# Kernel optimization log

Hardware: AMD Instinct MI355X
Metric: run time of the kernel (lower is better)

The kernel has to match this reference:

```python
import jax, jax.numpy as jnp
import numpy as np

CTX = 77; WIDTH = 512; HEADS = 8; LAYERS = 12; EMBED = 1024; VOCAB = 49408
N = 128; P = 8; LP = 16; EOT = 49407


def _ln(x, w, b, eps=1e-5):
    m = jnp.mean(x, axis=-1, keepdims=True)
    v = jnp.var(x, axis=-1, keepdims=True)
    return (x - m) * jax.lax.rsqrt(v + eps) * w + b


def setup_inputs() -> dict:
    key = jax.random.key(0)
    ks = jax.random.split(key, 12)
    # tokens strictly below EOT, then place exactly one EOT at a valid position (<= CTX-LP)
    text = jax.random.randint(ks[0], (N, CTX), 0, EOT)
    eot_pos = jax.random.randint(ks[1], (N,), 5, CTX - LP + 1)
    text = text.at[jnp.arange(N), eot_pos].set(EOT)
    s = 0.02
    return {
        "text": text,
        "context_prompt": jax.random.normal(ks[2], (P, LP, WIDTH)) * s,
        "tok_emb": jax.random.normal(ks[3], (VOCAB, WIDTH)) * s,
        "pos_emb": jax.random.normal(ks[4], (CTX, WIDTH)) * 0.01,
        "qkv_w": jax.random.normal(ks[5], (LAYERS, 3 * WIDTH, WIDTH)) * s,
        "qkv_b": jnp.zeros((LAYERS, 3 * WIDTH)),
        "out_w": jax.random.normal(ks[6], (LAYERS, WIDTH, WIDTH)) * s,
        "out_b": jnp.zeros((LAYERS, WIDTH)),
        "ln1_w": jnp.ones((LAYERS, WIDTH)),
        "ln1_b": jnp.zeros((LAYERS, WIDTH)),
        "ln2_w": jnp.ones((LAYERS, WIDTH)),
        "ln2_b": jnp.zeros((LAYERS, WIDTH)),
        "fc_w": jax.random.normal(ks[7], (LAYERS, 4 * WIDTH, WIDTH)) * s,
        "fc_b": jnp.zeros((LAYERS, 4 * WIDTH)),
        "proj_w": jax.random.normal(ks[8], (LAYERS, WIDTH, 4 * WIDTH)) * s,
        "proj_b": jnp.zeros((LAYERS, WIDTH)),
        "lnf_w": jnp.ones((WIDTH,)),
        "lnf_b": jnp.zeros((WIDTH,)),
        "text_projection": jax.random.normal(ks[9], (WIDTH, EMBED)) * s,
    }


def _encode(text, context_prompt, tok_emb, pos_emb, qkv_w, qkv_b, out_w, out_b,
            ln1_w, ln1_b, ln2_w, ln2_b, fc_w, fc_b, proj_w, proj_b,
            lnf_w, lnf_b, text_projection):
    pos_y = jnp.argmax(text == EOT, axis=1)                       # [N] first EOT per sample
    x = tok_emb[text]                                             # [N,L,D]
    t = jnp.arange(CTX)
    # vectorized per-sample insertion: out[t] = x[t] for t<pos_y; prompt[t-pos_y] for
    # pos_y<=t<pos_y+LP; x[t-LP+1] otherwise (matches the torch concat semantics)
    src = jnp.where(t[None] < pos_y[:, None], t[None], t[None] - LP + 1)
    src = jnp.clip(src, 0, CTX - 1)
    base = jnp.take_along_axis(x, src[:, :, None], axis=1)        # [N,L,D]
    in_prompt = (t[None] >= pos_y[:, None]) & (t[None] < pos_y[:, None] + LP)
    pidx = jnp.clip(t[None] - pos_y[:, None], 0, LP - 1)          # [N,L]
    prom = context_prompt[:, pidx, :]                             # [P,N,L,D]
    xn = jnp.where(in_prompt[None, :, :, None], prom, base[None]) + pos_emb
    B = P * N
    xn = xn.reshape(B, CTX, WIDTH)

    dh = WIDTH // HEADS
    scale = 1.0 / float(np.sqrt(dh))
    mask = jnp.triu(jnp.full((CTX, CTX), -jnp.inf, xn.dtype), 1)  # causal attn_mask

    def block(h, p):
        qw, qb, ow, ob, l1w, l1b, l2w, l2b, fw, fb, pw, pb = p
        y = _ln(h, l1w, l1b)
        qkv = y @ qw.T + qb
        q, k, v = jnp.split(qkv, 3, axis=-1)
        q = q.reshape(B, CTX, HEADS, dh)
        k = k.reshape(B, CTX, HEADS, dh)
        v = v.reshape(B, CTX, HEADS, dh)
        sc = jnp.einsum('blhd,bmhd->bhlm', q, k) * scale + mask
        a = jax.nn.softmax(sc, axis=-1)
        o = jnp.einsum('bhlm,bmhd->blhd', a, v).reshape(B, CTX, WIDTH)
        h = h + o @ ow.T + ob
        y = _ln(h, l2w, l2b)
        u = y @ fw.T + fb
        u = u * jax.nn.sigmoid(1.702 * u)                         # QuickGELU (CLIP)
        h = h + u @ pw.T + pb
        return h, None

    xn, _ = jax.lax.scan(block, xn, (qkv_w, qkv_b, out_w, out_b, ln1_w, ln1_b,
                                     ln2_w, ln2_b, fc_w, fc_b, proj_w, proj_b))
    xn = _ln(xn, lnf_w, lnf_b).reshape(P, N, CTX, WIDTH)
    take = (pos_y + LP - 1)[None, :, None, None]                  # shifted EOT position
    feats = jnp.take_along_axis(xn, jnp.broadcast_to(take, (P, N, 1, WIDTH)), axis=2)[:, :, 0, :]
    feats = feats @ text_projection                               # [P,N,E]
    feats = feats / jnp.linalg.norm(feats, axis=-1, keepdims=True)
    feats = jnp.mean(feats, axis=1, keepdims=True)                # [P,1,E]
    feats = feats / jnp.linalg.norm(feats, axis=-1, keepdims=True)
    return feats


def reference(text, context_prompt, tok_emb, pos_emb, qkv_w, qkv_b, out_w, out_b,
              ln1_w, ln1_b, ln2_w, ln2_b, fc_w, fc_b, proj_w, proj_b,
              lnf_w, lnf_b, text_projection):
    return _encode(text, context_prompt, tok_emb, pos_emb, qkv_w, qkv_b, out_w, out_b,
                   ln1_w, ln1_b, ln2_w, ln2_b, fc_w, fc_b, proj_w, proj_b,
                   lnf_w, lnf_b, text_projection)
```

## Files before the change

### kernel.cpp

```cpp
#include <hip/hip_runtime.h>
#include <math.h>
#include <stdint.h>

#define CTX 77
#define WIDTH 512
#define HEADS 8
#define DH 64
#define LAYERS 12
#define EMBED 1024
#define NTXT 128
#define PP 8
#define LPROMPT 16
#define EOTTOK 49407
#define BSEQ (PP*NTXT)
#define ROWS (BSEQ*CTX)

typedef unsigned short ushort_t;
typedef __attribute__((ext_vector_type(8))) short short8;
typedef __attribute__((ext_vector_type(4))) float floatx4;

__device__ __forceinline__ float b2f(ushort_t u){
  union { unsigned int i; float f; } x; x.i = ((unsigned int)u) << 16; return x.f;
}
__device__ __forceinline__ ushort_t f2b(float f){
  union { float f; unsigned int i; } x; x.f = f;
  unsigned int r = x.i + 0x7fffu + ((x.i >> 16) & 1u);
  return (ushort_t)(r >> 16);
}
__device__ __forceinline__ float wsum(float v){
  #pragma unroll
  for (int o = 32; o > 0; o >>= 1) v += __shfl_xor(v, o, 64);
  return v;
}
__device__ __forceinline__ float wmax(float v){
  #pragma unroll
  for (int o = 32; o > 0; o >>= 1) v = fmaxf(v, __shfl_xor(v, o, 64));
  return v;
}

__device__ __forceinline__ void async16(const void* g, void* l){
  __builtin_amdgcn_global_load_lds(
      (const __attribute__((address_space(1))) void*)(uintptr_t)g,
      (__attribute__((address_space(3))) void*)(uint32_t)(uintptr_t)l,
      16, 0, 0);
}

__global__ __launch_bounds__(256) void k_conv(
    const float* __restrict__ s, ushort_t* __restrict__ d, int n4)
{
  int i = blockIdx.x * 256 + threadIdx.x;
  if (i < n4){
    float4 v = ((const float4*)s)[i];
    ushort_t o[4] = { f2b(v.x), f2b(v.y), f2b(v.z), f2b(v.w) };
    ((int2*)d)[i] = *(int2*)o;
  }
}

__global__ void k_posy(const int* __restrict__ text, int* __restrict__ posy){
  int n = threadIdx.x;
  if (n < NTXT){
    int p = 0;
    for (int t = 0; t < CTX; ++t){ if (text[n*CTX + t] == EOTTOK){ p = t; break; } }
    posy[n] = p;
  }
}

template<bool RF32>
__global__ __launch_bounds__(256) void k_embed(
    const int* __restrict__ text, const float* __restrict__ cprompt,
    const float* __restrict__ tok_emb, const float* __restrict__ pos_emb,
    const int* __restrict__ posy, void* __restrict__ Hp)
{
  long long idx = (long long)blockIdx.x * 256 + threadIdx.x;
  int d   = (int)(idx & 511);
  int row = (int)(idx >> 9);
  int t  = row % CTX;
  int pn = row / CTX;
  int n  = pn % NTXT;
  int p  = pn / NTXT;
  int py = posy[n];
  float v;
  if (t >= py && t < py + LPROMPT){
    int pidx = t - py;
    v = cprompt[(p*LPROMPT + pidx)*WIDTH + d];
  } else {
    int src = (t < py) ? t : (t - LPROMPT + 1);
    src = min(max(src, 0), CTX-1);
    int tok = text[n*CTX + src];
    v = tok_emb[(long long)tok*WIDTH + d];
  }
  v += pos_emb[t*WIDTH + d];
  if constexpr (RF32) ((float*)Hp)[idx] = v;
  else                ((ushort_t*)Hp)[idx] = f2b(v);
}

template<bool RF32>
__global__ __launch_bounds__(256) void k_ln(
    const void* __restrict__ Hp, const float* __restrict__ w,
    const float* __restrict__ b, ushort_t* __restrict__ Y, int nrows)
{
  int wid = threadIdx.x >> 6, lane = threadIdx.x & 63;
  int row = blockIdx.x * 4 + wid;
  if (row >= nrows) return;
  float v[8];
  if constexpr (RF32){
    const float* x = (const float*)Hp + (long long)row * WIDTH;
    #pragma unroll
    for (int i = 0; i < 8; ++i) v[i] = x[lane*8 + i];
  } else {
    const ushort_t* x = (const ushort_t*)Hp + (long long)row * WIDTH;
    int4 raw = *(const int4*)(x + lane*8);
    ushort_t* u = (ushort_t*)&raw;
    #pragma unroll
    for (int i = 0; i < 8; ++i) v[i] = b2f(u[i]);
  }
  float s = 0.f, ss = 0.f;
  #pragma unroll
  for (int i = 0; i < 8; ++i){ s += v[i]; ss += v[i]*v[i]; }
  s = wsum(s); ss = wsum(ss);
  float mean = s * (1.0f/WIDTH);
  float var  = ss * (1.0f/WIDTH) - mean*mean;
  float rs = rsqrtf(var + 1e-5f);
  ushort_t o[8];
  #pragma unroll
  for (int i = 0; i < 8; ++i){
    int d = lane*8 + i;
    o[i] = f2b((v[i]-mean)*rs*w[d] + b[d]);
  }
  *(int4*)(Y + (long long)row*WIDTH + lane*8) = *(int4*)o;
}

template<int MODE, bool RF32>
__global__ __launch_bounds__(256) void k_gemm(
    const ushort_t* __restrict__ A, const ushort_t* __restrict__ W,
    const float* __restrict__ bias, void* __restrict__ Hp,
    ushort_t* __restrict__ O, int K, int N)
{
  __shared__ ushort_t As[128*64];
  __shared__ ushort_t Bs[128*64];
  int tid  = threadIdx.x;
  int lane = tid & 63, wid = tid >> 6;
  int wm = wid >> 1, wn = wid & 1;
  long long m0 = (long long)blockIdx.y * 128;
  int n0 = blockIdx.x * 128;

  floatx4 acc[4][4];
  #pragma unroll
  for (int i = 0; i < 4; ++i)
    #pragma unroll
    for (int j = 0; j < 4; ++j){ floatx4 z = {0.f,0.f,0.f,0.f}; acc[i][j] = z; }

  const int srow = tid >> 3;
  const int sc8  = ((tid ^ (tid >> 3)) & 7) * 8;
  const ushort_t* gA = A + (m0 + srow) * (long long)K + sc8;
  const ushort_t* gB = W + ((size_t)n0 + srow) * K + sc8;
  const size_t qstep = (size_t)32 * K;
  const int lbase = wid * 512;

  const int quad = lane >> 4, r = lane & 15;
  const int swz = (r & 7) * 8;

  for (int k0 = 0; k0 < K; k0 += 64){
    __syncthreads();
    #pragma unroll
    for (int q = 0; q < 4; ++q){
      async16(gA + q*qstep, As + q*2048 + lbase);
      async16(gB + q*qstep, Bs + q*2048 + lbase);
    }
    gA += 64; gB += 64;
    __syncthreads();
    #pragma unroll
    for (int s = 0; s < 2; ++s){
      const int co = (s*32 + quad*8) ^ swz;
      short8 af[4], bf[4];
      #pragma unroll
      for (int i = 0; i < 4; ++i) af[i] = *(const short8*)(As + (wm*64 + i*16 + r)*64 + co);
      #pragma unroll
      for (int j = 0; j < 4; ++j) bf[j] = *(const short8*)(Bs + (wn*64 + j*16 + r)*64 + co);
      #pragma unroll
      for (int i = 0; i < 4; ++i)
        #pragma unroll
        for (int j = 0; j < 4; ++j)
          acc[i][j] = __builtin_amdgcn_mfma_f32_16x16x32_bf16(af[i], bf[j], acc[i][j], 0, 0, 0);
    }
  }

  int cn = lane & 15;
  #pragma unroll
  for (int i = 0; i < 4; ++i){
    #pragma unroll
    for (int j = 0; j < 4; ++j){
      int gcol = n0 + wn*64 + j*16 + cn;
      float bv = bias[gcol];
      #pragma unroll
      for (int rg = 0; rg < 4; ++rg){
        long long grow = m0 + wm*64 + i*16 + quad*4 + rg;
        float v = acc[i][j][rg] + bv;
        if (MODE == 0){
          O[grow*N + gcol] = f2b(v);
        } else if (MODE == 1){
          float g = v / (1.0f + __expf(-1.702f*v));
          O[grow*N + gcol] = f2b(g);
        } else {
          long long idx = grow*N + gcol;
          if constexpr (RF32) ((float*)Hp)[idx] += v;
          else { ushort_t* hb = (ushort_t*)Hp; hb[idx] = f2b(b2f(hb[idx]) + v); }
        }
      }
    }
  }
}

__global__ __launch_bounds__(256) void k_attn(
    const ushort_t* __restrict__ QKV, ushort_t* __restrict__ Y)
{
  __shared__ char smem[55872];
  ushort_t* Qs = (ushort_t*)smem;
  ushort_t* Ks = (ushort_t*)(smem + 11520);
  float*    Ss = (float*)smem;
  ushort_t* Vt = (ushort_t*)(smem + 25920);
  ushort_t* Ps = (ushort_t*)(smem + 39232);

  int b = blockIdx.x >> 3, h = blockIdx.x & 7;
  int tid = threadIdx.x;
  int lane = tid & 63, wid = tid >> 6;
  int quad = lane >> 4, r = lane & 15;
  const ushort_t* base = QKV + (size_t)b*CTX*1536 + h*64;

  #pragma unroll
  for (int it = 0; it < 5; ++it){
    int id = tid + it*256;
    int t  = id >> 4;
    int d4 = (id & 15) * 4;
    ushort_t q[4], k[4], v[4];
    if (t < CTX){
      const ushort_t* rp = base + (size_t)t*1536 + d4;
      *(int2*)q = *(const int2*)(rp);
      *(int2*)k = *(const int2*)(rp + 512);
      *(int2*)v = *(const int2*)(rp + 1024);
    } else {
      q[0]=q[1]=q[2]=q[3]=0; k[0]=k[1]=k[2]=k[3]=0; v[0]=v[1]=v[2]=v[3]=0;
    }
    *(int2*)(Qs + t*72 + d4) = *(int2*)q;
    *(int2*)(Ks + t*72 + d4) = *(int2*)k;
    #pragma unroll
    for (int i = 0; i < 4; ++i) Vt[(d4+i)*104 + t] = v[i];
  }
  {
    int z = tid * 4;
    int d = z >> 4, c = 80 + (z & 15);
    ushort_t zz[4] = {0,0,0,0};
    *(int2*)(Vt + d*104 + c) = *(int2*)zz;
  }
  __syncthreads();

  const int TI[15] = {0,1,1,2,2,2,3,3,3,3,4,4,4,4,4};
  const int TJ[15] = {0,0,1,0,1,2,0,1,2,3,0,1,2,3,4};
  floatx4 cS[4];
  int ntile = 0;
  for (int tt = wid; tt < 15; tt += 4, ++ntile){
    int i = TI[tt], j = TJ[tt];
    floatx4 c = {0.f,0.f,0.f,0.f};
    #pragma unroll
    for (int s = 0; s < 2; ++s){
      short8 aq = *(const short8*)(Qs + (i*16 + r)*72 + s*32 + quad*8);
      short8 bk = *(const short8*)(Ks + (j*16 + r)*72 + s*32 + quad*8);
      c = __builtin_amdgcn_mfma_f32_16x16x32_bf16(aq, bk, c, 0, 0, 0);
    }
    cS[ntile] = c;
  }
  __syncthreads();

  {
    int idx = 0;
    for (int tt = wid; tt < 15; tt += 4, ++idx){
      int i = TI[tt], j = TJ[tt];
      #pragma unroll
      for (int rg = 0; rg < 4; ++rg){
        int q  = i*16 + quad*4 + rg;
        int kk = j*16 + r;
        float s = cS[idx][rg] * 0.125f;
        if (kk > q) s = -1e30f;
        Ss[q*81 + kk] = s;
      }
    }
  }
  __syncthreads();

  for (int q = wid; q < 80; q += 4){
    if (q >= CTX){
      Ps[q*104 + lane] = 0;
      if (lane < 32) Ps[q*104 + 64 + lane] = 0;
      continue;
    }
    int k1 = 64 + lane;
    float s0 = (lane <= q) ? Ss[q*81 + lane] : -1e30f;
    float s1 = (k1  <= q) ? Ss[q*81 + k1 ]  : -1e30f;
    float mx = wmax(fmaxf(s0, s1));
    float e0 = (lane <= q) ? __expf(s0 - mx) : 0.0f;
    float e1 = (k1  <= q) ? __expf(s1 - mx) : 0.0f;
    float inv = 1.0f / wsum(e0 + e1);
    Ps[q*104 + lane] = f2b(e0 * inv);
    if (lane < 32) Ps[q*104 + 64 + lane] = f2b(e1 * inv);
  }
  __syncthreads();

  for (int tt = wid; tt < 20; tt += 4){
    int mi = tt >> 2, ni = tt & 3;
    floatx4 c = {0.f,0.f,0.f,0.f};
    #pragma unroll
    for (int kc = 0; kc < 3; ++kc){
      short8 ap = *(const short8*)(Ps + (mi*16 + r)*104 + kc*32 + quad*8);
      short8 bv = *(const short8*)(Vt + (ni*16 + r)*104 + kc*32 + quad*8);
      c = __builtin_amdgcn_mfma_f32_16x16x32_bf16(ap, bv, c, 0, 0, 0);
    }
    #pragma unroll
    for (int rg = 0; rg < 4; ++rg){
      int q = mi*16 + quad*4 + rg;
      if (q < CTX)
        Y[((size_t)b*CTX + q)*WIDTH + h*64 + ni*16 + r] = f2b(c[rg]);
    }
  }
}

template<bool RF32>
__global__ __launch_bounds__(256) void k_lnf_gather(
    const void* __restrict__ Hp, const int* __restrict__ posy,
    const float* __restrict__ w, const float* __restrict__ b,
    ushort_t* __restrict__ FI)
{
  int wid = threadIdx.x >> 6, lane = threadIdx.x & 63;
  int rr = blockIdx.x * 4 + wid;
  if (rr >= BSEQ) return;
  int n = rr % NTXT;
  int tok = posy[n] + LPROMPT - 1;
  long long row = (long long)rr*CTX + tok;
  float v[8];
  if constexpr (RF32){
    const float* x = (const float*)Hp + row * WIDTH;
    #pragma unroll
    for (int i = 0; i < 8; ++i) v[i] = x[lane*8 + i];
  } else {
    const ushort_t* x = (const ushort_t*)Hp + row * WIDTH;
    int4 raw = *(const int4*)(x + lane*8);
    ushort_t* u = (ushort_t*)&raw;
    #pragma unroll
    for (int i = 0; i < 8; ++i) v[i] = b2f(u[i]);
  }
  float s = 0.f, ss = 0.f;
  #pragma unroll
  for (int i = 0; i < 8; ++i){ s += v[i]; ss += v[i]*v[i]; }
  s = wsum(s); ss = wsum(ss);
  float mean = s * (1.0f/WIDTH);
  float var  = ss * (1.0f/WIDTH) - mean*mean;
  float rs = rsqrtf(var + 1e-5f);
  ushort_t o[8];
  #pragma unroll
  for (int i = 0; i < 8; ++i){
    int d = lane*8 + i;
    o[i] = f2b((v[i]-mean)*rs*w[d] + b[d]);
  }
  *(int4*)(FI + (long long)rr*WIDTH + lane*8) = *(int4*)o;
}

__global__ __launch_bounds__(256) void k_fproj(
    const ushort_t* __restrict__ FI, const float* __restrict__ TP,
    float* __restrict__ F)
{
  int idx = blockIdx.x * 256 + threadIdx.x;
  int e = idx & (EMBED-1);
  int m = idx >> 10;
  float acc = 0.f;
  #pragma unroll 8
  for (int k = 0; k < WIDTH; ++k)
    acc += b2f(FI[m*WIDTH + k]) * TP[k*EMBED + e];
  F[idx] = acc;
}

__global__ __launch_bounds__(256) void k_rownorm(float* __restrict__ F)
{
  __shared__ float red[4];
  int rr = blockIdx.x;
  float* x = F + (long long)rr*EMBED;
  float ss = 0.f;
  for (int i = threadIdx.x; i < EMBED; i += 256){ float v = x[i]; ss += v*v; }
  ss = wsum(ss);
  int wid = threadIdx.x >> 6, lane = threadIdx.x & 63;
  if (lane == 0) red[wid] = ss;
  __syncthreads();
  float inv = rsqrtf(red[0]+red[1]+red[2]+red[3]);
  for (int i = threadIdx.x; i < EMBED; i += 256) x[i] *= inv;
}

__global__ __launch_bounds__(256) void k_meannorm(
    const float* __restrict__ F, float* __restrict__ OUT)
{
  __shared__ float red[4];
  int p = blockIdx.x;
  float m[4]; float ss = 0.f;
  #pragma unroll
  for (int j = 0; j < 4; ++j){
    int e = threadIdx.x + j*256;
    float s = 0.f;
    for (int n = 0; n < NTXT; ++n) s += F[((long long)(p*NTXT + n))*EMBED + e];
    s *= (1.0f/NTXT);
    m[j] = s; ss += s*s;
  }
  ss = wsum(ss);
  int wid = threadIdx.x >> 6, lane = threadIdx.x & 63;
  if (lane == 0) red[wid] = ss;
  __syncthreads();
  float inv = rsqrtf(red[0]+red[1]+red[2]+red[3]);
  #pragma unroll
  for (int j = 0; j < 4; ++j)
    OUT[p*EMBED + threadIdx.x + j*256] = m[j]*inv;
}


template<bool RF32>
static void run_all(const int* text, const float* cprompt, const float* tok_emb,
                    const float* pos_emb,
                    const ushort_t* Wqkv, const float* qkv_b,
                    const ushort_t* Wout, const float* out_b,
                    const float* ln1_w, const float* ln1_b,
                    const float* ln2_w, const float* ln2_b,
                    const ushort_t* Wfc, const float* fc_b,
                    const ushort_t* Wproj, const float* proj_b,
                    const float* lnf_w, const float* lnf_b, const float* tproj,
                    int* posy, void* H, ushort_t* Y, ushort_t* BIG,
                    ushort_t* FI, float* F, float* OUT, int sc, hipStream_t stream)
{
  const int rows_c = ROWS / sc;
  const int seqs_c = BSEQ / sc;

  k_posy<<<1, 128, 0, stream>>>(text, posy);
  k_embed<RF32><<<(ROWS*512)/256, 256, 0, stream>>>(text, cprompt, tok_emb, pos_emb, posy, H);

  for (int L = 0; L < LAYERS; ++L){
    k_ln<RF32><<<ROWS/4, 256, 0, stream>>>(H, ln1_w + L*WIDTH, ln1_b + L*WIDTH, Y, ROWS);
    for (int c = 0; c < sc; ++c){
      size_t r0 = (size_t)c * rows_c;
      k_gemm<0,RF32><<<dim3(12, rows_c/128), 256, 0, stream>>>(
          Y + r0*WIDTH, Wqkv + (size_t)L*1536*512, qkv_b + L*1536,
          nullptr, BIG, 512, 1536);
      k_attn<<<seqs_c*HEADS, 256, 0, stream>>>(BIG, Y + r0*WIDTH);
    }
    k_gemm<2,RF32><<<dim3(4, ROWS/128), 256, 0, stream>>>(
        Y, Wout + (size_t)L*512*512, out_b + L*512, H, nullptr, 512, 512);
    k_ln<RF32><<<ROWS/4, 256, 0, stream>>>(H, ln2_w + L*WIDTH, ln2_b + L*WIDTH, Y, ROWS);
    for (int c = 0; c < sc; ++c){
      size_t r0 = (size_t)c * rows_c;
      void* Hoff = RF32 ? (void*)((float*)H + r0*WIDTH) : (void*)((ushort_t*)H + r0*WIDTH);
      k_gemm<1,RF32><<<dim3(16, rows_c/128), 256, 0, stream>>>(
          Y + r0*WIDTH, Wfc + (size_t)L*2048*512, fc_b + L*2048,
          nullptr, BIG, 512, 2048);
      k_gemm<2,RF32><<<dim3(4, rows_c/128), 256, 0, stream>>>(
          BIG, Wproj + (size_t)L*512*2048, proj_b + L*512, Hoff, nullptr, 2048, 512);
    }
  }

  k_lnf_gather<RF32><<<BSEQ/4, 256, 0, stream>>>(H, posy, lnf_w, lnf_b, FI);
  k_fproj<<<(BSEQ*EMBED)/256, 256, 0, stream>>>(FI, tproj, F);
  k_rownorm<<<BSEQ, 256, 0, stream>>>(F);
  k_meannorm<<<PP, 256, 0, stream>>>(F, OUT);
}

extern "C" void kernel_launch(void* const* d_in, const int* in_sizes, int n_in,
                              void* d_out, int out_size, void* d_ws, size_t ws_size,
                              hipStream_t stream)
{
  const int*   text    = (const int*)d_in[0];
  const float* cprompt = (const float*)d_in[1];
  const float* tok_emb = (const float*)d_in[2];
  const float* pos_emb = (const float*)d_in[3];
  const float* qkv_w   = (const float*)d_in[4];
  const float* qkv_b   = (const float*)d_in[5];
  const float* out_w   = (const float*)d_in[6];
  const float* out_b   = (const float*)d_in[7];
  const float* ln1_w   = (const float*)d_in[8];
  const float* ln1_b   = (const float*)d_in[9];
  const float* ln2_w   = (const float*)d_in[10];
  const float* ln2_b   = (const float*)d_in[11];
  const float* fc_w    = (const float*)d_in[12];
  const float* fc_b    = (const float*)d_in[13];
  const float* proj_w  = (const float*)d_in[14];
  const float* proj_b  = (const float*)d_in[15];
  const float* lnf_w   = (const float*)d_in[16];
  const float* lnf_b   = (const float*)d_in[17];
  const float* tproj   = (const float*)d_in[18];

  const size_t nQKV = (size_t)LAYERS*1536*512;
  const size_t nOUT = (size_t)LAYERS*512*512;
  const size_t nFC  = (size_t)LAYERS*2048*512;
  const size_t nPRJ = (size_t)LAYERS*512*2048;
  const size_t nWB  = nQKV + nOUT + nFC + nPRJ;

  auto al = [](size_t b){ return (b + 255) & ~(size_t)255; };
  const size_t fixed = al(NTXT*sizeof(int)) + al((size_t)ROWS*WIDTH*2 )
                     + al((size_t)BSEQ*WIDTH*2 ) + al((size_t)BSEQ*EMBED*4 )
                     + al(nWB*2);
  int sc = 8; bool hf32 = false;
  const int scs[4] = {1, 2, 4, 8};
  bool found = false;
  for (int pass = 0; pass < 2 && !found; ++pass){
    size_t hbytes = (size_t)ROWS*WIDTH*(pass == 0 ? 4 : 2);
    for (int i = 0; i < 4; ++i){
      size_t big = (size_t)(ROWS/scs[i]) * 2048 * 2;
      if (fixed + al(hbytes) + al(big) <= ws_size){
        sc = scs[i]; hf32 = (pass == 0); found = true; break;
      }
    }
  }

  char* ws = (char*)d_ws;
  size_t off = 0;
  auto alloc = [&](size_t bytes)->char*{
    char* pp = ws + off; off += (bytes + 255) & ~(size_t)255; return pp;
  };
  int*      posy = (int*)     alloc(NTXT*sizeof(int));
  void*     H    = (void*)    alloc((size_t)ROWS*WIDTH*(hf32 ? 4 : 2));
  ushort_t* Y    = (ushort_t*)alloc((size_t)ROWS*WIDTH*2);
  ushort_t* BIG  = (ushort_t*)alloc((size_t)(ROWS/sc)*2048*2);
  ushort_t* FI   = (ushort_t*)alloc((size_t)BSEQ*WIDTH*2);
  float*    F    = (float*)   alloc((size_t)BSEQ*EMBED*4);
  ushort_t* WB   = (ushort_t*)alloc(nWB*2);
  ushort_t* Wqkv = WB;
  ushort_t* Wout = WB + nQKV;
  ushort_t* Wfc  = WB + nQKV + nOUT;
  ushort_t* Wprj = WB + nQKV + nOUT + nFC;

  k_conv<<<(int)((nQKV/4 + 255)/256), 256, 0, stream>>>(qkv_w,  Wqkv, (int)(nQKV/4));
  k_conv<<<(int)((nOUT/4 + 255)/256), 256, 0, stream>>>(out_w,  Wout, (int)(nOUT/4));
  k_conv<<<(int)((nFC /4 + 255)/256), 256, 0, stream>>>(fc_w,   Wfc,  (int)(nFC /4));
  k_conv<<<(int)((nPRJ/4 + 255)/256), 256, 0, stream>>>(proj_w, Wprj, (int)(nPRJ/4));

  if (hf32)
    run_all<true >(text, cprompt, tok_emb, pos_emb, Wqkv, qkv_b, Wout, out_b,
                   ln1_w, ln1_b, ln2_w, ln2_b, Wfc, fc_b, Wprj, proj_b,
                   lnf_w, lnf_b, tproj, posy, H, Y, BIG, FI, F,
                   (float*)d_out, sc, stream);
  else
    run_all<false>(text, cprompt, tok_emb, pos_emb, Wqkv, qkv_b, Wout, out_b,
                   ln1_w, ln1_b, ln2_w, ln2_b, Wfc, fc_b, Wprj, proj_b,
                   lnf_w, lnf_b, tproj, posy, H, Y, BIG, FI, F,
                   (float*)d_out, sc, stream);
}
```

Baseline: 17.50 ms.

## Vectorize embedding, shrink attention LDS, add occupancy hints, force chunked scheduling

The embedding kernel now has each thread handle eight contiguous elements using float4 loads and wide stores instead of one scalar element per thread. The attention kernel's score buffer is packed to a 77-column stride and padding rows are no longer written, which reduces LDS use so more blocks can fit per CU (launch bounds now request 3). The GEMM gets a min-blocks-per-CU launch bound of 4, which may force register limits and spills. Workspace selection now allows only 4 or 8 sequence chunks, so the intermediate buffer stays smaller and more cache-resident, at the cost of more kernel launches.

Result: faster. 15.05 ms (-14.0%).

```diff
diff --git a/kernel.cpp b/kernel.cpp
--- a/kernel.cpp
+++ b/kernel.cpp
@@ -72,26 +72,41 @@
     const int* __restrict__ posy, void* __restrict__ Hp)
 {
   long long idx = (long long)blockIdx.x * 256 + threadIdx.x;
-  int d   = (int)(idx & 511);
-  int row = (int)(idx >> 9);
+  int d8  = (int)(idx & 63) * 8;
+  int row = (int)(idx >> 6);
   int t  = row % CTX;
   int pn = row / CTX;
   int n  = pn % NTXT;
   int p  = pn / NTXT;
   int py = posy[n];
-  float v;
+  const float* src;
   if (t >= py && t < py + LPROMPT){
-    int pidx = t - py;
-    v = cprompt[(p*LPROMPT + pidx)*WIDTH + d];
+    src = cprompt + ((p*LPROMPT + (t - py))*WIDTH + d8);
   } else {
-    int src = (t < py) ? t : (t - LPROMPT + 1);
-    src = min(max(src, 0), CTX-1);
-    int tok = text[n*CTX + src];
-    v = tok_emb[(long long)tok*WIDTH + d];
-  }
-  v += pos_emb[t*WIDTH + d];
-  if constexpr (RF32) ((float*)Hp)[idx] = v;
-  else                ((ushort_t*)Hp)[idx] = f2b(v);
+    int s0 = (t < py) ? t : (t - LPROMPT + 1);
+    s0 = min(max(s0, 0), CTX-1);
+    int tok = text[n*CTX + s0];
+    src = tok_emb + ((long long)tok*WIDTH + d8);
+  }
+  const float* pe = pos_emb + (t*WIDTH + d8);
+  float4 a0 = *(const float4*)(src);
+  float4 a1 = *(const float4*)(src + 4);
+  float4 b0 = *(const float4*)(pe);
+  float4 b1 = *(const float4*)(pe + 4);
+  float v[8] = { a0.x+b0.x, a0.y+b0.y, a0.z+b0.z, a0.w+b0.w,
+                 a1.x+b1.x, a1.y+b1.y, a1.z+b1.z, a1.w+b1.w };
+  long long base = (long long)row*WIDTH + d8;
+  if constexpr (RF32){
+    float4 o0 = {v[0],v[1],v[2],v[3]};
+    float4 o1 = {v[4],v[5],v[6],v[7]};
+    *(float4*)((float*)Hp + base)     = o0;
+    *(float4*)((float*)Hp + base + 4) = o1;
+  } else {
+    ushort_t o[8];
+    #pragma unroll
+    for (int i = 0; i < 8; ++i) o[i] = f2b(v[i]);
+    *(int4*)((ushort_t*)Hp + base) = *(int4*)o;
+  }
 }
 
 template<bool RF32>
@@ -131,7 +146,7 @@
 }
 
 template<int MODE, bool RF32>
-__global__ __launch_bounds__(256) void k_gemm(
+__global__ __launch_bounds__(256, 4) void k_gemm(
     const ushort_t* __restrict__ A, const ushort_t* __restrict__ W,
     const float* __restrict__ bias, void* __restrict__ Hp,
     ushort_t* __restrict__ O, int K, int N)
@@ -211,15 +226,15 @@
   }
 }
 
-__global__ __launch_bounds__(256) void k_attn(
+__global__ __launch_bounds__(256, 3) void k_attn(
     const ushort_t* __restrict__ QKV, ushort_t* __restrict__ Y)
 {
-  __shared__ char smem[55872];
+  __shared__ char smem[53056];
   ushort_t* Qs = (ushort_t*)smem;
-  ushort_t* Ks = (ushort_t*)(smem + 11520);
+  ushort_t* Ks = (ushort_t*)(smem + 11088);
   float*    Ss = (float*)smem;
-  ushort_t* Vt = (ushort_t*)(smem + 25920);
-  ushort_t* Ps = (ushort_t*)(smem + 39232);
+  ushort_t* Vt = (ushort_t*)(smem + 23728);
+  ushort_t* Ps = (ushort_t*)(smem + 37040);
 
   int b = blockIdx.x >> 3, h = blockIdx.x & 7;
   int tid = threadIdx.x;
@@ -238,11 +253,11 @@
       *(int2*)q = *(const int2*)(rp);
       *(int2*)k = *(const int2*)(rp + 512);
       *(int2*)v = *(const int2*)(rp + 1024);
+      *(int2*)(Qs + t*72 + d4) = *(int2*)q;
+      *(int2*)(Ks + t*72 + d4) = *(int2*)k;
     } else {
-      q[0]=q[1]=q[2]=q[3]=0; k[0]=k[1]=k[2]=k[3]=0; v[0]=v[1]=v[2]=v[3]=0;
-    }
-    *(int2*)(Qs + t*72 + d4) = *(int2*)q;
-    *(int2*)(Ks + t*72 + d4) = *(int2*)k;
+      v[0]=v[1]=v[2]=v[3]=0;
+    }
     #pragma unroll
     for (int i = 0; i < 4; ++i) Vt[(d4+i)*104 + t] = v[i];
   }
@@ -281,21 +296,16 @@
         int kk = j*16 + r;
         float s = cS[idx][rg] * 0.125f;
         if (kk > q) s = -1e30f;
-        Ss[q*81 + kk] = s;
+        if (q < CTX && kk < CTX) Ss[q*77 + kk] = s;
       }
     }
   }
   __syncthreads();
 
-  for (int q = wid; q < 80; q += 4){
-    if (q >= CTX){
-      Ps[q*104 + lane] = 0;
-      if (lane < 32) Ps[q*104 + 64 + lane] = 0;
-      continue;
-    }
+  for (int q = wid; q < CTX; q += 4){
     int k1 = 64 + lane;
-    float s0 = (lane <= q) ? Ss[q*81 + lane] : -1e30f;
-    float s1 = (k1  <= q) ? Ss[q*81 + k1 ]  : -1e30f;
+    float s0 = (lane <= q) ? Ss[q*77 + lane] : -1e30f;
+    float s1 = (k1  <= q) ? Ss[q*77 + k1 ]  : -1e30f;
     float mx = wmax(fmaxf(s0, s1));
     float e0 = (lane <= q) ? __expf(s0 - mx) : 0.0f;
     float e1 = (k1  <= q) ? __expf(s1 - mx) : 0.0f;
@@ -307,10 +317,11 @@
 
   for (int tt = wid; tt < 20; tt += 4){
     int mi = tt >> 2, ni = tt & 3;
+    int arow = min(mi*16 + r, CTX-1);
     floatx4 c = {0.f,0.f,0.f,0.f};
     #pragma unroll
     for (int kc = 0; kc < 3; ++kc){
-      short8 ap = *(const short8*)(Ps + (mi*16 + r)*104 + kc*32 + quad*8);
+      short8 ap = *(const short8*)(Ps + arow*104 + kc*32 + quad*8);
       short8 bv = *(const short8*)(Vt + (ni*16 + r)*104 + kc*32 + quad*8);
       c = __builtin_amdgcn_mfma_f32_16x16x32_bf16(ap, bv, c, 0, 0, 0);
     }
@@ -434,7 +445,7 @@
   const int seqs_c = BSEQ / sc;
 
   k_posy<<<1, 128, 0, stream>>>(text, posy);
-  k_embed<RF32><<<(ROWS*512)/256, 256, 0, stream>>>(text, cprompt, tok_emb, pos_emb, posy, H);
+  k_embed<RF32><<<(ROWS*64)/256, 256, 0, stream>>>(text, cprompt, tok_emb, pos_emb, posy, H);
 
   for (int L = 0; L < LAYERS; ++L){
     k_ln<RF32><<<ROWS/4, 256, 0, stream>>>(H, ln1_w + L*WIDTH, ln1_b + L*WIDTH, Y, ROWS);
@@ -500,11 +511,11 @@
                      + al((size_t)BSEQ*WIDTH*2 ) + al((size_t)BSEQ*EMBED*4 )
                      + al(nWB*2);
   int sc = 8; bool hf32 = false;
-  const int scs[4] = {1, 2, 4, 8};
+  const int scs[2] = {4, 8};
   bool found = false;
   for (int pass = 0; pass < 2 && !found; ++pass){
     size_t hbytes = (size_t)ROWS*WIDTH*(pass == 0 ? 4 : 2);
-    for (int i = 0; i < 4; ++i){
+    for (int i = 0; i < 2; ++i){
       size_t big = (size_t)(ROWS/scs[i]) * 2048 * 2;
       if (fixed + al(hbytes) + al(big) <= ws_size){
         sc = scs[i]; hf32 = (pass == 0); found = true; break;
```
